# Optimization experiments

Hardware: AMD Instinct MI355X
Metric: run time of the kernel (lower is better)

## Reference

```python
import jax, jax.numpy as jnp
import numpy as np

D = 128; H = 8; L = 6; DFF = 512; EPS = 1e-5; ETA = 1e-3; MAXLEN = 5000


def layernorm(x, g, b):
    m = jnp.mean(x, -1, keepdims=True)
    v = jnp.mean((x - m) ** 2, -1, keepdims=True)
    return (x - m) / jnp.sqrt(v + EPS) * g + b


def mha(q_in, kv_in, Wi, bi, Wo, bo):
    # Wi: [3D, D] packed q/k/v projections (torch in_proj layout)
    dh = D // H
    q = q_in @ Wi[:D].T + bi[:D]
    k = kv_in @ Wi[D:2 * D].T + bi[D:2 * D]
    v = kv_in @ Wi[2 * D:].T + bi[2 * D:]
    B_, Lq, _ = q.shape
    Lk = k.shape[1]
    q = q.reshape(B_, Lq, H, dh)
    k = k.reshape(B_, Lk, H, dh)
    v = v.reshape(B_, Lk, H, dh)
    att = jax.nn.softmax(jnp.einsum('bqhd,bkhd->bhqk', q, k) / jnp.sqrt(jnp.asarray(dh, q.dtype)), axis=-1)
    o = jnp.einsum('bhqk,bkhd->bqhd', att, v).reshape(B_, Lq, D)
    return o @ Wo.T + bo


def posenc(x):
    pos = jnp.arange(MAXLEN, dtype=x.dtype)[:, None]
    div = jnp.exp(jnp.arange(0, D, 2, dtype=x.dtype) * (-jnp.log(jnp.asarray(10000.0, x.dtype)) / D))
    pe = jnp.zeros((MAXLEN, D), x.dtype).at[:, 0::2].set(jnp.sin(pos * div)).at[:, 1::2].set(jnp.cos(pos * div))
    # faithful to original: slices pe by x.size(0) which is the BATCH dim (batch_first tensors)
    return x + pe[: x.shape[0], None, :]


def reference(src, tgt, emb, femb_w, femb_b,
              enc_inw, enc_inb, enc_ow, enc_ob, enc_l1g, enc_l1b, enc_l2g, enc_l2b,
              enc_f1w, enc_f1b, enc_f2w, enc_f2b, enc_ng, enc_nb,
              dec_inw, dec_inb, dec_ow, dec_ob, dec_cinw, dec_cinb, dec_cow, dec_cob,
              dec_l1g, dec_l1b, dec_l2g, dec_l2b, dec_l3g, dec_l3b,
              dec_f1w, dec_f1b, dec_f2w, dec_f2b, dec_ng, dec_nb, fc_w, fc_b):
    scale = jnp.sqrt(jnp.asarray(D, jnp.float32))
    s = posenc(emb[src] * scale)                     # [B,S,D]
    t = posenc((tgt @ femb_w.T + femb_b) * scale)    # [B,T,D]
    mem = s
    for i in range(L):  # encoder (post-norm, ReLU, dropout=0 in eval)
        a = mha(mem, mem, enc_inw[i], enc_inb[i], enc_ow[i], enc_ob[i])
        mem = layernorm(mem + a, enc_l1g[i], enc_l1b[i])
        f = jax.nn.relu(mem @ enc_f1w[i].T + enc_f1b[i]) @ enc_f2w[i].T + enc_f2b[i]
        mem = layernorm(mem + f, enc_l2g[i], enc_l2b[i])
    mem = layernorm(mem, enc_ng, enc_nb)
    y = t
    for i in range(L):  # decoder
        a = mha(y, y, dec_inw[i], dec_inb[i], dec_ow[i], dec_ob[i])
        y = layernorm(y + a, dec_l1g[i], dec_l1b[i])
        c = mha(y, mem, dec_cinw[i], dec_cinb[i], dec_cow[i], dec_cob[i])
        y = layernorm(y + c, dec_l2g[i], dec_l2b[i])
        f = jax.nn.relu(y @ dec_f1w[i].T + dec_f1b[i]) @ dec_f2w[i].T + dec_f2b[i]
        y = layernorm(y + f, dec_l3g[i], dec_l3b[i])
    y = layernorm(y, dec_ng, dec_nb)
    out = y @ fc_w.T + fc_b  # [B,T,1]
    # nn-corrected TN parameter vector: vec + eta * nn_output (pre-final-contract)
    return tgt[..., 0] + ETA * out[..., 0]


def setup_inputs():
    B, S, T = 4, 100, 2048
    ks = iter(jax.random.split(jax.random.key(0), 64))

    def w(shape, s=0.02):
        return jax.random.normal(next(ks), shape, jnp.float32) * s

    inp = {}
    inp['src'] = jax.random.randint(next(ks), (B, S), 0, 2)
    inp['tgt'] = jax.random.normal(next(ks), (B, T, 1), jnp.float32)
    inp['emb'] = w((2, D), 1.0)
    inp['femb_w'] = w((D, 1)); inp['femb_b'] = jnp.zeros((D,))
    inp['enc_inw'] = w((L, 3 * D, D)); inp['enc_inb'] = jnp.zeros((L, 3 * D))
    inp['enc_ow'] = w((L, D, D)); inp['enc_ob'] = jnp.zeros((L, D))
    inp['enc_l1g'] = jnp.ones((L, D)); inp['enc_l1b'] = jnp.zeros((L, D))
    inp['enc_l2g'] = jnp.ones((L, D)); inp['enc_l2b'] = jnp.zeros((L, D))
    inp['enc_f1w'] = w((L, DFF, D)); inp['enc_f1b'] = jnp.zeros((L, DFF))
    inp['enc_f2w'] = w((L, D, DFF)); inp['enc_f2b'] = jnp.zeros((L, D))
    inp['enc_ng'] = jnp.ones((D,)); inp['enc_nb'] = jnp.zeros((D,))
    inp['dec_inw'] = w((L, 3 * D, D)); inp['dec_inb'] = jnp.zeros((L, 3 * D))
    inp['dec_ow'] = w((L, D, D)); inp['dec_ob'] = jnp.zeros((L, D))
    inp['dec_cinw'] = w((L, 3 * D, D)); inp['dec_cinb'] = jnp.zeros((L, 3 * D))
    inp['dec_cow'] = w((L, D, D)); inp['dec_cob'] = jnp.zeros((L, D))
    inp['dec_l1g'] = jnp.ones((L, D)); inp['dec_l1b'] = jnp.zeros((L, D))
    inp['dec_l2g'] = jnp.ones((L, D)); inp['dec_l2b'] = jnp.zeros((L, D))
    inp['dec_l3g'] = jnp.ones((L, D)); inp['dec_l3b'] = jnp.zeros((L, D))
    inp['dec_f1w'] = w((L, DFF, D)); inp['dec_f1b'] = jnp.zeros((L, DFF))
    inp['dec_f2w'] = w((L, D, DFF)); inp['dec_f2b'] = jnp.zeros((L, D))
    inp['dec_ng'] = jnp.ones((D,)); inp['dec_nb'] = jnp.zeros((D,))
    inp['fc_w'] = w((1, D)); inp['fc_b'] = jnp.zeros((1,))
    return inp
```

## Files before the change

### kernel.cpp

```cpp
#include <hip/hip_runtime.h>
#include <hip/hip_bf16.h>
#include <math.h>

#define B_ 4
#define S_ 100
#define T_ 2048
#define DM 128
#define NH 8
#define DH 16
#define NL 6
#define DFFN 512

#define SQRT_D 11.313708498984761f
#define LN10K  9.210340371976184f
#define QSCALE 0.36067376022224085f

typedef _Float16 v4h __attribute__((ext_vector_type(4)));
typedef _Float16 v8h __attribute__((ext_vector_type(8)));
typedef float    v4f __attribute__((ext_vector_type(4)));

__device__ __forceinline__ float fexp2(float x) { return __builtin_amdgcn_exp2f(x); }

__device__ __forceinline__ v4f mfma16(v4h a, v4h b, v4f c) {
    return __builtin_amdgcn_mfma_f32_16x16x16f16(a, b, c, 0, 0, 0);
}

__device__ __forceinline__ void gload_lds16(const void* g, void* l) {
    __builtin_amdgcn_global_load_lds(
        (const __attribute__((address_space(1))) unsigned int*)g,
        (__attribute__((address_space(3))) unsigned int*)l, 16, 0, 0);
}

__device__ __forceinline__ float pe_val(int pos, int d) {
    int i = d >> 1;
    float dv = __expf((float)i * (-2.0f * LN10K / 128.0f));
    float ang = (float)pos * dv;
    return (d & 1) ? __cosf(ang) : __sinf(ang);
}

__global__ __launch_bounds__(256) void conv_w(
    const float* __restrict__ p0, const float* __restrict__ p1,
    const float* __restrict__ p2, const float* __restrict__ p3,
    const float* __restrict__ p4, const float* __restrict__ p5,
    const float* __restrict__ p6, const float* __restrict__ p7,
    const float* __restrict__ p8, const float* __restrict__ p9,
    _Float16* __restrict__ out)
{
    int seg = blockIdx.y;
    const float* s; int sz; long off;
    switch (seg) {
        case 0: s = p0; sz = 294912; off = 0;       break;
        case 1: s = p1; sz = 98304;  off = 294912;  break;
        case 2: s = p2; sz = 393216; off = 393216;  break;
        case 3: s = p3; sz = 393216; off = 786432;  break;
        case 4: s = p4; sz = 294912; off = 1179648; break;
        case 5: s = p5; sz = 98304;  off = 1474560; break;
        case 6: s = p6; sz = 294912; off = 1572864; break;
        case 7: s = p7; sz = 98304;  off = 1867776; break;
        case 8: s = p8; sz = 393216; off = 1966080; break;
        default: s = p9; sz = 393216; off = 2359296; break;
    }
    int idx = (blockIdx.x * 256 + threadIdx.x) * 4;
    if (idx >= sz) return;
    float4 v = *(const float4*)(s + idx);
    v4h h = { (_Float16)v.x, (_Float16)v.y, (_Float16)v.z, (_Float16)v.w };
    *(v4h*)(out + off + idx) = h;
}

__global__ __launch_bounds__(256) void embed_src_kernel(
    const int* __restrict__ src, const float* __restrict__ emb,
    _Float16* __restrict__ outh)
{
    int idx = blockIdx.x * 256 + threadIdx.x;
    if (idx >= B_ * S_ * DM) return;
    int d = idx & 127;
    int row = idx >> 7;
    int b = row / S_;
    int tok = src[row];
    float v = emb[tok * DM + d] * SQRT_D + pe_val(b, d);
    outh[idx] = (_Float16)v;
}

__global__ __launch_bounds__(256) void embed_tgt_kernel(
    const float* __restrict__ tgt, const float* __restrict__ fw,
    const float* __restrict__ fb, _Float16* __restrict__ outh)
{
    int idx = blockIdx.x * 256 + threadIdx.x;
    if (idx >= B_ * T_ * DM) return;
    int d = idx & 127;
    int row = idx >> 7;
    int b = row >> 11;
    float v = (tgt[row] * fw[d] + fb[d]) * SQRT_D + pe_val(b, d);
    outh[idx] = (_Float16)v;
}

template<int MODE>
__global__ __launch_bounds__(256) void gemm_h(
    const _Float16* __restrict__ A, const _Float16* __restrict__ W,
    const float* __restrict__ bias,
    _Float16* __restrict__ Ch,
    _Float16* __restrict__ qo, _Float16* __restrict__ ko, _Float16* __restrict__ vo,
    int M, int N, int K, int L, int Lkp, int part_off, int Lshift,
    long zws, int zbs, long zks, long zvs)
{
    if (MODE == 2) {
        int zi = blockIdx.z;
        W += (size_t)zi * zws;
        bias += (size_t)zi * zbs;
        ko += (size_t)zi * zks;
        vo += (size_t)zi * zvs;
    }
    __shared__ _Float16 As[128][72];
    __shared__ _Float16 Ws[64][72];
    const int t = threadIdx.x;
    const int wave = t >> 6, lane = t & 63;
    const int col16 = lane & 15, grp = lane >> 4;
    const int row0 = blockIdx.x * 128, col0 = blockIdx.y * 64;
    const int wrow0 = (wave >> 1) * 64, wcol0 = (wave & 1) * 32;

    v4f acc[4][2];
    #pragma unroll
    for (int m = 0; m < 4; m++)
        #pragma unroll
        for (int n = 0; n < 2; n++) acc[m][n] = (v4f){0.f, 0.f, 0.f, 0.f};

    for (int k0 = 0; k0 < K; k0 += 64) {
        #pragma unroll
        for (int i = 0; i < 4; i++) {
            int id = i * 256 + t;
            int r = id >> 3, j = id & 7;
            int gr = min(row0 + r, M - 1);
            int4 v = *(const int4*)(A + (size_t)gr * K + k0 + j * 8);
            *(int4*)&As[r][j * 8] = v;
        }
        #pragma unroll
        for (int i = 0; i < 2; i++) {
            int id = i * 256 + t;
            int r = id >> 3, j = id & 7;
            int4 v = *(const int4*)(W + (size_t)(col0 + r) * K + k0 + j * 8);
            *(int4*)&Ws[r][j * 8] = v;
        }
        __syncthreads();
        #pragma unroll
        for (int kk = 0; kk < 4; kk++) {
            v4h a[4], bf[2];
            #pragma unroll
            for (int m = 0; m < 4; m++)
                a[m] = *(const v4h*)&As[wrow0 + m * 16 + col16][kk * 16 + grp * 4];
            #pragma unroll
            for (int n = 0; n < 2; n++)
                bf[n] = *(const v4h*)&Ws[wcol0 + n * 16 + col16][kk * 16 + grp * 4];
            #pragma unroll
            for (int m = 0; m < 4; m++)
                #pragma unroll
                for (int n = 0; n < 2; n++)
                    acc[m][n] = mfma16(a[m], bf[n], acc[m][n]);
        }
        __syncthreads();
    }

    #pragma unroll
    for (int n = 0; n < 2; n++) {
        int gcol = col0 + wcol0 + n * 16 + col16;
        float bv = bias[gcol];
        #pragma unroll
        for (int m = 0; m < 4; m++) {
            int rbase = row0 + wrow0 + m * 16 + grp * 4;
            #pragma unroll
            for (int r = 0; r < 4; r++) {
                int grow = rbase + r;
                if (grow >= M) continue;
                float v = acc[m][n][r] + bv;
                int pc = gcol + part_off;
                int part = pc >> 7;
                int h = (pc >> 4) & 7;
                int d = pc & 15;
                int b = Lshift ? (grow >> Lshift) : (grow / L);
                int pos = grow - b * L;
                int bh = b * NH + h;
                if (part == 0)
                    qo[((size_t)bh * L + pos) * 16 + d] = (_Float16)(v * QSCALE);
                else if (part == 1)
                    ko[((size_t)bh * L + pos) * 16 + d] = (_Float16)v;
                else
                    vo[((size_t)bh * 16 + d) * Lkp + pos] = (_Float16)v;
            }
        }
    }
}

template<int CROSS>
__global__ __launch_bounds__(128) void post_ln(
    const _Float16* __restrict__ A,
    const _Float16* __restrict__ po, const float* __restrict__ pm, const float* __restrict__ pl,
    const _Float16* __restrict__ Wo1, const float* __restrict__ bo1,
    const _Float16* __restrict__ resg,
    const float* __restrict__ g1, const float* __restrict__ bt1,
    const _Float16* __restrict__ Wq, const float* __restrict__ bq,
    const _Float16* __restrict__ KC_l, const _Float16* __restrict__ VC_l,
    const _Float16* __restrict__ Wo2, const float* __restrict__ bo2,
    const float* __restrict__ g2, const float* __restrict__ bt2,
    const _Float16* __restrict__ W1, const float* __restrict__ fb1,
    const _Float16* __restrict__ W2, const float* __restrict__ fb2,
    const float* __restrict__ g3, const float* __restrict__ bt3,
    _Float16* __restrict__ yout, int M)
{
    __shared__ _Float16 As[32][136];
    __shared__ _Float16 Ws[128][132];
    __shared__ _Float16 YL[32][136];
    __shared__ _Float16 QS[32][136];
    __shared__ _Float16 Khs[2][2048];
    __shared__ _Float16 Vhs[2][2048];
    __shared__ _Float16 W1s[64][136];
    __shared__ _Float16 Hs[32][72];
    __shared__ _Float16 W2s[128][72];
    const int t = threadIdx.x;
    const int wave = t >> 6, lane = t & 63;
    const int col16 = lane & 15, grp = lane >> 4;
    const int row0 = blockIdx.x * 32;
    const int rl = wave * 16 + grp * 4;

    v4f acc[8];
    #pragma unroll
    for (int n = 0; n < 8; n++) acc[n] = (v4f){0.f, 0.f, 0.f, 0.f};
    #pragma unroll
    for (int i = 0; i < 4; i++) {
        int id = i * 128 + t;
        int r = id >> 4, j = id & 15;
        int grow = min(row0 + r, M - 1);
        if (CROSS) {
            int dim0 = j * 8;
            int h = dim0 >> 4;
            int doff = dim0 & 8;
            int b = grow >> 11, q = grow & 2047;
            size_t i0 = ((size_t)(b * 2 + 0) * NH + h) * T_ + q;
            size_t i1 = ((size_t)(b * 2 + 1) * NH + h) * T_ + q;
            float m0 = pm[i0], m1 = pm[i1];
            float MM = fmaxf(m0, m1);
            float w0 = fexp2(m0 - MM) * pl[i0];
            float w1 = fexp2(m1 - MM) * pl[i1];
            float inv = 1.0f / (w0 + w1);
            w0 *= inv; w1 *= inv;
            v8h o0 = *(const v8h*)&po[i0 * 16 + doff];
            v8h o1 = *(const v8h*)&po[i1 * 16 + doff];
            v8h mrg;
            #pragma unroll
            for (int e = 0; e < 8; e++)
                mrg[e] = (_Float16)((float)o0[e] * w0 + (float)o1[e] * w1);
            *(v8h*)&As[r][j * 8] = mrg;
        } else {
            int4 v = *(const int4*)(A + (size_t)grow * DM + j * 8);
            *(int4*)&As[r][j * 8] = v;
        }
    }
    #pragma unroll
    for (int i = 0; i < 16; i++) {
        int id = i * 128 + t;
        int r = id >> 4, j = id & 15;
        int4 v = *(const int4*)(Wo1 + (size_t)r * DM + j * 8);
        *(int4*)&Ws[r][j * 8] = v;
    }
    __syncthreads();
    #pragma unroll
    for (int kk = 0; kk < 8; kk++) {
        v4h a = *(const v4h*)&As[wave * 16 + col16][kk * 16 + grp * 4];
        #pragma unroll
        for (int n = 0; n < 8; n++) {
            v4h bf = *(const v4h*)&Ws[n * 16 + col16][kk * 16 + grp * 4];
            acc[n] = mfma16(a, bf, acc[n]);
        }
    }
    {
        float bv[8], gv[8], btv[8];
        #pragma unroll
        for (int n = 0; n < 8; n++) {
            bv[n] = bo1[col16 + 16 * n];
            gv[n] = g1[col16 + 16 * n];
            btv[n] = bt1[col16 + 16 * n];
        }
        #pragma unroll
        for (int r = 0; r < 4; r++) {
            int grow = min(row0 + rl + r, M - 1);
            float x[8];
            float sum = 0.f;
            #pragma unroll
            for (int n = 0; n < 8; n++) {
                x[n] = acc[n][r] + bv[n] + (float)resg[(size_t)grow * DM + col16 + 16 * n];
                sum += x[n];
            }
            sum += __shfl_xor(sum, 1, 64);
            sum += __shfl_xor(sum, 2, 64);
            sum += __shfl_xor(sum, 4, 64);
            sum += __shfl_xor(sum, 8, 64);
            float mean = sum * (1.0f / 128.0f);
            float vs = 0.f;
            #pragma unroll
            for (int n = 0; n < 8; n++) { x[n] -= mean; vs += x[n] * x[n]; }
            vs += __shfl_xor(vs, 1, 64);
            vs += __shfl_xor(vs, 2, 64);
            vs += __shfl_xor(vs, 4, 64);
            vs += __shfl_xor(vs, 8, 64);
            float rstd = rsqrtf(vs * (1.0f / 128.0f) + 1e-5f);
            #pragma unroll
            for (int n = 0; n < 8; n++)
                YL[rl + r][col16 + 16 * n] = (_Float16)(x[n] * rstd * gv[n] + btv[n]);
        }
    }
    __syncthreads();

    if (CROSS) {
        v4f qacc[8];
        #pragma unroll
        for (int n = 0; n < 8; n++) qacc[n] = (v4f){0.f, 0.f, 0.f, 0.f};
        #pragma unroll
        for (int i = 0; i < 16; i++) {
            int id = i * 128 + t;
            int r = id >> 4, j = id & 15;
            int4 v = *(const int4*)(Wq + (size_t)r * DM + j * 8);
            *(int4*)&Ws[r][j * 8] = v;
        }
        __syncthreads();
        #pragma unroll
        for (int kk = 0; kk < 8; kk++) {
            v4h a = *(const v4h*)&YL[wave * 16 + col16][kk * 16 + grp * 4];
            #pragma unroll
            for (int n = 0; n < 8; n++) {
                v4h bf = *(const v4h*)&Ws[n * 16 + col16][kk * 16 + grp * 4];
                qacc[n] = mfma16(a, bf, qacc[n]);
            }
        }
        __syncthreads();
        #pragma unroll
        for (int n = 0; n < 8; n++) {
            float bb = bq[n * 16 + col16];
            #pragma unroll
            for (int r = 0; r < 4; r++)
                QS[rl + r][n * 16 + col16] = (_Float16)((qacc[n][r] + bb) * QSCALE);
        }

        const int b = row0 >> 11;
        const char* kbB = (const char*)(KC_l + (size_t)(b * NH) * S_ * DH);
        const char* vbB = (const char*)(VC_l + (size_t)(b * NH) * DH * 128);
        for (int h = 0; h < NH; h += 2) {
            __syncthreads();
            #pragma unroll
            for (int s = 0; s < 2; s++) {
                int hh = h + s;
                #pragma unroll
                for (int rd = 0; rd < 2; rd++) {
                    int dstB = rd * 2048 + wave * 1024 + lane * 16;
                    int krow = dstB >> 5;
                    int half = (dstB >> 4) & 1;
                    gload_lds16(kbB + (long)hh * 3200 + (long)krow * 32 +
                                ((half ^ ((krow >> 2) & 1)) << 4),
                                (char*)&Khs[s][0] + rd * 2048 + wave * 1024);
                }
                #pragma unroll
                for (int rd = 0; rd < 2; rd++) {
                    int dstB = rd * 2048 + wave * 1024 + lane * 16;
                    int vd = dstB >> 8;
                    int inoff = dstB & 255;
                    gload_lds16(vbB + (long)hh * 4096 + (long)vd * 256 +
                                (inoff ^ ((vd & 7) << 4)),
                                (char*)&Vhs[s][0] + rd * 2048 + wave * 1024);
                }
            }
            __syncthreads();

            #pragma unroll
            for (int s = 0; s < 2; s++) {
                int hh = h + s;
                v4h q_frag = *(const v4h*)&QS[wave * 16 + col16][hh * 16 + grp * 4];
                const int kxor = (col16 & 4) << 2;
                v4f s4[7];
                #pragma unroll
                for (int sub = 0; sub < 7; sub++) {
                    int koff = ((sub * 16 + col16) << 5) + ((grp * 8) ^ kxor);
                    v4h k_frag = *(const v4h*)((const char*)&Khs[s][0] + koff);
                    s4[sub] = mfma16(k_frag, q_frag, (v4f){0.f, 0.f, 0.f, 0.f});
                }
                #pragma unroll
                for (int r = 0; r < 4; r++) {
                    int key = 96 + grp * 4 + r;
                    if (key >= S_) s4[6][r] = -1e30f;
                }
                float mx = -1e30f;
                #pragma unroll
                for (int sub = 0; sub < 7; sub++)
                    #pragma unroll
                    for (int r = 0; r < 4; r++) mx = fmaxf(mx, s4[sub][r]);
                mx = fmaxf(mx, __shfl_xor(mx, 16, 64));
                mx = fmaxf(mx, __shfl_xor(mx, 32, 64));
                float l = 0.f;
                float p[7][4];
                #pragma unroll
                for (int sub = 0; sub < 7; sub++)
                    #pragma unroll
                    for (int r = 0; r < 4; r++) {
                        p[sub][r] = fexp2(s4[sub][r] - mx);
                        l += p[sub][r];
                    }
                l += __shfl_xor(l, 16, 64);
                l += __shfl_xor(l, 32, 64);
                float inv = 1.0f / l;
                v4f o = {0.f, 0.f, 0.f, 0.f};
                #pragma unroll
                for (int sub = 0; sub < 7; sub++) {
                    v4h ph = { (_Float16)(p[sub][0] * inv), (_Float16)(p[sub][1] * inv),
                               (_Float16)(p[sub][2] * inv), (_Float16)(p[sub][3] * inv) };
                    int vbyte = (col16 << 8) + ((sub * 32 + grp * 8) ^ ((col16 & 7) << 4));
                    v4h vt = *(const v4h*)((const char*)&Vhs[s][0] + vbyte);
                    o = mfma16(vt, ph, o);
                }
                #pragma unroll
                for (int r = 0; r < 4; r++)
                    QS[wave * 16 + col16][hh * 16 + grp * 4 + r] = (_Float16)o[r];
            }
        }
        __syncthreads();

        v4f ac2[8];
        #pragma unroll
        for (int n = 0; n < 8; n++) ac2[n] = (v4f){0.f, 0.f, 0.f, 0.f};
        #pragma unroll
        for (int i = 0; i < 16; i++) {
            int id = i * 128 + t;
            int r = id >> 4, j = id & 15;
            int4 v = *(const int4*)(Wo2 + (size_t)r * DM + j * 8);
            *(int4*)&Ws[r][j * 8] = v;
        }
        __syncthreads();
        #pragma unroll
        for (int kk = 0; kk < 8; kk++) {
            v4h a = *(const v4h*)&QS[wave * 16 + col16][kk * 16 + grp * 4];
            #pragma unroll
            for (int n = 0; n < 8; n++) {
                v4h bf = *(const v4h*)&Ws[n * 16 + col16][kk * 16 + grp * 4];
                ac2[n] = mfma16(a, bf, ac2[n]);
            }
        }
        {
            float bv[8], gv[8], btv[8];
            #pragma unroll
            for (int n = 0; n < 8; n++) {
                bv[n] = bo2[col16 + 16 * n];
                gv[n] = g2[col16 + 16 * n];
                btv[n] = bt2[col16 + 16 * n];
            }
            #pragma unroll
            for (int r = 0; r < 4; r++) {
                float x[8];
                float sum = 0.f;
                #pragma unroll
                for (int n = 0; n < 8; n++) {
                    x[n] = ac2[n][r] + bv[n] + (float)YL[rl + r][col16 + 16 * n];
                    sum += x[n];
                }
                sum += __shfl_xor(sum, 1, 64);
                sum += __shfl_xor(sum, 2, 64);
                sum += __shfl_xor(sum, 4, 64);
                sum += __shfl_xor(sum, 8, 64);
                float mean = sum * (1.0f / 128.0f);
                float vs = 0.f;
                #pragma unroll
                for (int n = 0; n < 8; n++) { x[n] -= mean; vs += x[n] * x[n]; }
                vs += __shfl_xor(vs, 1, 64);
                vs += __shfl_xor(vs, 2, 64);
                vs += __shfl_xor(vs, 4, 64);
                vs += __shfl_xor(vs, 8, 64);
                float rstd = rsqrtf(vs * (1.0f / 128.0f) + 1e-5f);
                #pragma unroll
                for (int n = 0; n < 8; n++)
                    YL[rl + r][col16 + 16 * n] = (_Float16)(x[n] * rstd * gv[n] + btv[n]);
            }
        }
        __syncthreads();
    }

    v4f oacc[8];
    #pragma unroll
    for (int n = 0; n < 8; n++) oacc[n] = (v4f){0.f, 0.f, 0.f, 0.f};
    for (int hc = 0; hc < 8; hc++) {
        #pragma unroll
        for (int rd = 0; rd < 8; rd++) {
            int id = rd * 128 + t;
            int r = id >> 4, j = id & 15;
            int4 v = *(const int4*)(W1 + (size_t)(hc * 64 + r) * DM + j * 8);
            *(int4*)&W1s[r][j * 8] = v;
        }
        #pragma unroll
        for (int rd = 0; rd < 8; rd++) {
            int id = rd * 128 + t;
            int r = id >> 3, j = id & 7;
            int4 v = *(const int4*)(W2 + (size_t)r * DFFN + hc * 64 + j * 8);
            *(int4*)&W2s[r][j * 8] = v;
        }
        __syncthreads();
        v4f hacc[4];
        #pragma unroll
        for (int n = 0; n < 4; n++) hacc[n] = (v4f){0.f, 0.f, 0.f, 0.f};
        #pragma unroll
        for (int kk = 0; kk < 8; kk++) {
            v4h a = *(const v4h*)&YL[wave * 16 + col16][kk * 16 + grp * 4];
            #pragma unroll
            for (int n = 0; n < 4; n++) {
                v4h bf = *(const v4h*)&W1s[n * 16 + col16][kk * 16 + grp * 4];
                hacc[n] = mfma16(a, bf, hacc[n]);
            }
        }
        #pragma unroll
        for (int n = 0; n < 4; n++) {
            float bb = fb1[hc * 64 + n * 16 + col16];
            #pragma unroll
            for (int r = 0; r < 4; r++) {
                float h = fmaxf(hacc[n][r] + bb, 0.f);
                Hs[rl + r][n * 16 + col16] = (_Float16)h;
            }
        }
        #pragma unroll
        for (int kk = 0; kk < 4; kk++) {
            v4h a = *(const v4h*)&Hs[wave * 16 + col16][kk * 16 + grp * 4];
            #pragma unroll
            for (int n = 0; n < 8; n++) {
                v4h bf = *(const v4h*)&W2s[n * 16 + col16][kk * 16 + grp * 4];
                oacc[n] = mfma16(a, bf, oacc[n]);
            }
        }
        __syncthreads();
    }
    {
        float bv[8], gv[8], btv[8];
        #pragma unroll
        for (int n = 0; n < 8; n++) {
            bv[n] = fb2[col16 + 16 * n];
            gv[n] = g3[col16 + 16 * n];
            btv[n] = bt3[col16 + 16 * n];
        }
        #pragma unroll
        for (int r = 0; r < 4; r++) {
            int row = row0 + rl + r;
            float x[8];
            float sum = 0.f;
            #pragma unroll
            for (int n = 0; n < 8; n++) {
                x[n] = oacc[n][r] + bv[n] + (float)YL[rl + r][col16 + 16 * n];
                sum += x[n];
            }
            sum += __shfl_xor(sum, 1, 64);
            sum += __shfl_xor(sum, 2, 64);
            sum += __shfl_xor(sum, 4, 64);
            sum += __shfl_xor(sum, 8, 64);
            float mean = sum * (1.0f / 128.0f);
            float vs = 0.f;
            #pragma unroll
            for (int n = 0; n < 8; n++) { x[n] -= mean; vs += x[n] * x[n]; }
            vs += __shfl_xor(vs, 1, 64);
            vs += __shfl_xor(vs, 2, 64);
            vs += __shfl_xor(vs, 4, 64);
            vs += __shfl_xor(vs, 8, 64);
            float rstd = rsqrtf(vs * (1.0f / 128.0f) + 1e-5f);
            if (row < M) {
                #pragma unroll
                for (int n = 0; n < 8; n++) {
                    float o = x[n] * rstd * gv[n] + btv[n];
                    yout[(size_t)row * DM + col16 + 16 * n] = (_Float16)o;
                }
            }
        }
    }
}

template<int FINAL>
__global__ __launch_bounds__(256, 6) void attn_p3(
    const _Float16* __restrict__ qh, const _Float16* __restrict__ kh,
    const _Float16* __restrict__ vth, _Float16* __restrict__ outh,
    _Float16* __restrict__ po, float* __restrict__ pm, float* __restrict__ pl,
    int Lq, int Lk, int Lkp, int NS)
{
    __shared__ _Float16 KV[2][2048];
    const int zb = blockIdx.z;
    const int b = zb / NS, split = zb - b * NS;
    const int h = blockIdx.y;
    const int wave = threadIdx.x >> 6, lane = threadIdx.x & 63;
    const int col16 = lane & 15, grp = lane >> 4;
    const int bh = b * NH + h;
    const int qrow = (blockIdx.x * 4 + wave) * 16 + col16;
    const int qcl = min(qrow, Lq - 1);

    v4h q_frag = *(const v4h*)(qh + ((size_t)bh * Lq + qcl) * 16 + grp * 4);
    const char* kbB = (const char*)(kh + (size_t)bh * Lk * 16);
    const char* vbB = (const char*)(vth + (size_t)bh * 16 * Lkp);
    const int LkpB = Lkp * 2;

    const int kvLen = Lk / NS;
    const int kv0 = split * kvLen;
    const int kvEnd = kv0 + kvLen;

    const int krow = wave * 32 + (lane >> 1);
    const long ksrc_off = (long)krow * 32 + (((lane & 1) ^ ((krow >> 2) & 1)) << 4);
    const int vd = (wave & 1) * 8 + (lane >> 3);
    const long vsrc_off = (long)vd * LkpB + (((lane & 7) * 16) ^ ((vd & 7) << 4));
    char* ldsK = (char*)&KV[0][0] + wave * 1024;
    char* ldsV = (char*)&KV[0][0] + 2048 + (wave & 1) * 1024;

    auto stage = [&](int buf, int kc) {
        if (wave < 2)
            gload_lds16(kbB + (long)kc * 32 + ksrc_off, ldsK + buf * 4096);
        else
            gload_lds16(vbB + (long)kc * 2 + vsrc_off, ldsV + buf * 4096);
    };

    const int kxor = (col16 & 4) << 2;

    float m = -1e30f;
    v4f l4 = {0.f, 0.f, 0.f, 0.f};
    v4f oa = {0.f, 0.f, 0.f, 0.f}, ob = {0.f, 0.f, 0.f, 0.f};

    stage(0, kv0);
    __syncthreads();

    int nChunks = (kvLen + 63) >> 6;
    int cur = 0;
    for (int ci = 0; ci < nChunks; ci++, cur ^= 1) {
        int kc = kv0 + ci * 64;
        if (ci + 1 < nChunks) stage(cur ^ 1, kc + 64);

        const char* base = (const char*)&KV[cur][0];
        v4f s4[4];
        #pragma unroll
        for (int sub = 0; sub < 4; sub++) {
            int koff = ((sub * 16 + col16) << 5) + ((grp * 8) ^ kxor);
            v4h k_frag = *(const v4h*)(base + koff);
            s4[sub] = mfma16(k_frag, q_frag, (v4f){0.f, 0.f, 0.f, 0.f});
        }
        if (kc + 64 > kvEnd) {
            #pragma unroll
            for (int sub = 0; sub < 4; sub++)
                #pragma unroll
                for (int r = 0; r < 4; r++) {
                    int key = kc + sub * 16 + grp * 4 + r;
                    if (key >= kvEnd) s4[sub][r] = -1e30f;
                }
        }
        float c0 = fmaxf(fmaxf(s4[0][0], s4[0][1]), fmaxf(s4[0][2], s4[0][3]));
        float c1 = fmaxf(fmaxf(s4[1][0], s4[1][1]), fmaxf(s4[1][2], s4[1][3]));
        float c2 = fmaxf(fmaxf(s4[2][0], s4[2][1]), fmaxf(s4[2][2], s4[2][3]));
        float c3 = fmaxf(fmaxf(s4[3][0], s4[3][1]), fmaxf(s4[3][2], s4[3][3]));
        float cm = fmaxf(fmaxf(c0, c1), fmaxf(c2, c3));
        if (__any(cm > m + 8.0f)) {
            float nm = fmaxf(cm, m);
            nm = fmaxf(nm, __shfl_xor(nm, 16, 64));
            nm = fmaxf(nm, __shfl_xor(nm, 32, 64));
            float corr = fexp2(m - nm);
            l4[0] *= corr; l4[1] *= corr; l4[2] *= corr; l4[3] *= corr;
            oa[0] *= corr; oa[1] *= corr; oa[2] *= corr; oa[3] *= corr;
            ob[0] *= corr; ob[1] *= corr; ob[2] *= corr; ob[3] *= corr;
            m = nm;
        }
        v4h ph[4];
        #pragma unroll
        for (int sub = 0; sub < 4; sub++) {
            float p0 = fexp2(s4[sub][0] - m);
            float p1 = fexp2(s4[sub][1] - m);
            float p2 = fexp2(s4[sub][2] - m);
            float p3 = fexp2(s4[sub][3] - m);
            l4[0] += p0; l4[1] += p1; l4[2] += p2; l4[3] += p3;
            ph[sub] = (v4h){ (_Float16)p0, (_Float16)p1, (_Float16)p2, (_Float16)p3 };
        }
        #pragma unroll
        for (int sub = 0; sub < 4; sub++) {
            int vbyte = 2048 + (col16 << 7) + ((sub * 32 + grp * 8) ^ ((col16 & 7) << 4));
            v4h vt_frag = *(const v4h*)(base + vbyte);
            if (sub & 2)
                ob = mfma16(vt_frag, ph[sub], ob);
            else
                oa = mfma16(vt_frag, ph[sub], oa);
        }
        __syncthreads();
    }

    float l = (l4[0] + l4[1]) + (l4[2] + l4[3]);
    l += __shfl_xor(l, 16, 64);
    l += __shfl_xor(l, 32, 64);
    float inv = 1.0f / l;
    v4f o_acc = {oa[0] + ob[0], oa[1] + ob[1], oa[2] + ob[2], oa[3] + ob[3]};
    if (qrow < Lq) {
        v4h ov = { (_Float16)(o_acc[0] * inv), (_Float16)(o_acc[1] * inv),
                   (_Float16)(o_acc[2] * inv), (_Float16)(o_acc[3] * inv) };
        if (FINAL) {
            *(v4h*)(outh + ((size_t)b * Lq + qrow) * DM + h * DH + grp * 4) = ov;
        } else {
            size_t pidx = ((size_t)zb * NH + h) * Lq + qrow;
            *(v4h*)(po + pidx * 16 + grp * 4) = ov;
            if (grp == 0) { pm[pidx] = m; pl[pidx] = l; }
        }
    }
}

__global__ __launch_bounds__(256) void ln_h(
    _Float16* __restrict__ y, const float* __restrict__ g,
    const float* __restrict__ bta, int M)
{
    int row = blockIdx.x * 4 + (threadIdx.x >> 6);
    int lane = threadIdx.x & 63;
    if (row >= M) return;
    _Float16* yr = y + (size_t)row * DM;
    float x0 = (float)yr[lane], x1 = (float)yr[lane + 64];
    float sum = x0 + x1;
    #pragma unroll
    for (int off = 32; off > 0; off >>= 1) sum += __shfl_xor(sum, off, 64);
    float mean = sum * (1.0f / 128.0f);
    float d0 = x0 - mean, d1 = x1 - mean;
    float vs = d0 * d0 + d1 * d1;
    #pragma unroll
    for (int off = 32; off > 0; off >>= 1) vs += __shfl_xor(vs, off, 64);
    float rstd = rsqrtf(vs * (1.0f / 128.0f) + 1e-5f);
    yr[lane]      = (_Float16)(d0 * rstd * g[lane]      + bta[lane]);
    yr[lane + 64] = (_Float16)(d1 * rstd * g[lane + 64] + bta[lane + 64]);
}

__global__ __launch_bounds__(256) void final_ln_kernel(
    const _Float16* __restrict__ y, const float* __restrict__ tgt,
    const float* __restrict__ g, const float* __restrict__ bta,
    const float* __restrict__ fcw, const float* __restrict__ fcb,
    float* __restrict__ out)
{
    int row = blockIdx.x * 4 + (threadIdx.x >> 6);
    int lane = threadIdx.x & 63;
    const _Float16* yr = y + (size_t)row * DM;
    float x0 = (float)yr[lane], x1 = (float)yr[lane + 64];
    float sum = x0 + x1;
    #pragma unroll
    for (int off = 32; off > 0; off >>= 1) sum += __shfl_xor(sum, off, 64);
    float mean = sum * (1.0f / 128.0f);
    float d0 = x0 - mean, d1 = x1 - mean;
    float vs = d0 * d0 + d1 * d1;
    #pragma unroll
    for (int off = 32; off > 0; off >>= 1) vs += __shfl_xor(vs, off, 64);
    float rstd = rsqrtf(vs * (1.0f / 128.0f) + 1e-5f);
    float o0 = d0 * rstd * g[lane]      + bta[lane];
    float o1 = d1 * rstd * g[lane + 64] + bta[lane + 64];
    float a = o0 * fcw[lane] + o1 * fcw[lane + 64];
    #pragma unroll
    for (int off = 32; off > 0; off >>= 1) a += __shfl_xor(a, off, 64);
    if (lane == 0) out[row] = tgt[row] + 1.0e-3f * (a + fcb[0]);
}

extern "C" void kernel_launch(void* const* d_in, const int* in_sizes, int n_in,
                              void* d_out, int out_size, void* d_ws, size_t ws_size,
                              hipStream_t stream)
{
    (void)in_sizes; (void)n_in; (void)out_size; (void)ws_size;
    const int*   src     = (const int*)  d_in[0];
    const float* tgt     = (const float*)d_in[1];
    const float* emb     = (const float*)d_in[2];
    const float* femb_w  = (const float*)d_in[3];
    const float* femb_b  = (const float*)d_in[4];
    const float* enc_inw = (const float*)d_in[5];
    const float* enc_inb = (const float*)d_in[6];
    const float* enc_ow  = (const float*)d_in[7];
    const float* enc_ob  = (const float*)d_in[8];
    const float* enc_l1g = (const float*)d_in[9];
    const float* enc_l1b = (const float*)d_in[10];
    const float* enc_l2g = (const float*)d_in[11];
    const float* enc_l2b = (const float*)d_in[12];
    const float* enc_f1w = (const float*)d_in[13];
    const float* enc_f1b = (const float*)d_in[14];
    const float* enc_f2w = (const float*)d_in[15];
    const float* enc_f2b = (const float*)d_in[16];
    const float* enc_ng  = (const float*)d_in[17];
    const float* enc_nb  = (const float*)d_in[18];
    const float* dec_inw = (const float*)d_in[19];
    const float* dec_inb = (const float*)d_in[20];
    const float* dec_ow  = (const float*)d_in[21];
    const float* dec_ob  = (const float*)d_in[22];
    const float* dec_cinw= (const float*)d_in[23];
    const float* dec_cinb= (const float*)d_in[24];
    const float* dec_cow = (const float*)d_in[25];
    const float* dec_cob = (const float*)d_in[26];
    const float* dec_l1g = (const float*)d_in[27];
    const float* dec_l1b = (const float*)d_in[28];
    const float* dec_l2g = (const float*)d_in[29];
    const float* dec_l2b = (const float*)d_in[30];
    const float* dec_l3g = (const float*)d_in[31];
    const float* dec_l3b = (const float*)d_in[32];
    const float* dec_f1w = (const float*)d_in[33];
    const float* dec_f1b = (const float*)d_in[34];
    const float* dec_f2w = (const float*)d_in[35];
    const float* dec_f2b = (const float*)d_in[36];
    const float* dec_ng  = (const float*)d_in[37];
    const float* dec_nb  = (const float*)d_in[38];
    const float* fc_w    = (const float*)d_in[39];
    const float* fc_b    = (const float*)d_in[40];

    float* ws = (float*)d_ws;
    float* pm   = ws;
    float* pl   = ws + 131072;
    _Float16* hb = (_Float16*)(ws + 262144);
    _Float16* mem_h  = hb;
    _Float16* ybuf_h = hb + 51200;
    _Float16* aout_h = hb + 1099776;
    _Float16* wh     = hb + 2148352;
    _Float16* po     = hb + 4900864;
    _Float16* QH     = hb + 11192320;
    _Float16* KH     = hb + 12240896;
    _Float16* VTH    = hb + 13289472;
    _Float16* KC     = hb + 14338048;
    _Float16* VC     = hb + 14645248;

    const long W_ENC_INW = 0,       W_ENC_OW = 294912,  W_ENC_F1W = 393216,  W_ENC_F2W = 786432;
    const long W_DEC_INW = 1179648, W_DEC_OW = 1474560, W_DEC_CINW = 1572864, W_DEC_COW = 1867776;
    const long W_DEC_F1W = 1966080, W_DEC_F2W = 2359296;

    conv_w<<<dim3(384, 10), 256, 0, stream>>>(enc_inw, enc_ow, enc_f1w, enc_f2w,
                                              dec_inw, dec_ow, dec_cinw, dec_cow,
                                              dec_f1w, dec_f2w, wh);

    embed_src_kernel<<<200, 256, 0, stream>>>(src, emb, mem_h);
    for (int i = 0; i < NL; i++) {
        gemm_h<2><<<dim3(4, 6), 256, 0, stream>>>(mem_h, wh + W_ENC_INW + i * 49152, enc_inb + i * 384,
            nullptr, QH, KH, VTH, 400, 384, 128, 100, 128, 0, 0, 0, 0, 0, 0);
        attn_p3<1><<<dim3(2, NH, B_), 256, 0, stream>>>(QH, KH, VTH, aout_h,
            nullptr, nullptr, nullptr, 100, 100, 128, 1);
        post_ln<0><<<13, 128, 0, stream>>>(aout_h,
            nullptr, nullptr, nullptr,
            wh + W_ENC_OW + i * 16384, enc_ob + i * 128,
            mem_h, enc_l1g + i * 128, enc_l1b + i * 128,
            nullptr, nullptr, nullptr, nullptr, nullptr, nullptr, nullptr, nullptr,
            wh + W_ENC_F1W + i * 65536, enc_f1b + i * 512,
            wh + W_ENC_F2W + i * 65536, enc_f2b + i * 128,
            enc_l2g + i * 128, enc_l2b + i * 128,
            mem_h, 400);
    }
    ln_h<<<100, 256, 0, stream>>>(mem_h, enc_ng, enc_nb, 400);
    gemm_h<2><<<dim3(4, 4, 6), 256, 0, stream>>>(mem_h, wh + W_DEC_CINW + 16384, dec_cinb + 128,
        nullptr, nullptr, KC, VC, 400, 256, 128, 100, 128, 128, 0,
        49152, 384, 51200, 65536);

    embed_tgt_kernel<<<4096, 256, 0, stream>>>(tgt, femb_w, femb_b, ybuf_h);
    for (int i = 0; i < NL; i++) {
        gemm_h<2><<<dim3(64, 6), 256, 0, stream>>>(ybuf_h, wh + W_DEC_INW + i * 49152, dec_inb + i * 384,
            nullptr, QH, KH, VTH, 8192, 384, 128, 2048, 2048, 0, 11, 0, 0, 0, 0);
        attn_p3<0><<<dim3(32, NH, B_ * 2), 256, 0, stream>>>(QH, KH, VTH, nullptr,
            po, pm, pl, 2048, 2048, 2048, 2);
        post_ln<1><<<256, 128, 0, stream>>>(nullptr,
            po, pm, pl,
            wh + W_DEC_OW + i * 16384, dec_ob + i * 128,
            ybuf_h, dec_l1g + i * 128, dec_l1b + i * 128,
            wh + W_DEC_CINW + i * 49152, dec_cinb + i * 384,
            KC + i * 51200, VC + i * 65536,
            wh + W_DEC_COW + i * 16384, dec_cob + i * 128,
            dec_l2g + i * 128, dec_l2b + i * 128,
            wh + W_DEC_F1W + i * 65536, dec_f1b + i * 512,
            wh + W_DEC_F2W + i * 65536, dec_f2b + i * 128,
            dec_l3g + i * 128, dec_l3b + i * 128,
            ybuf_h, 8192);
    }
    final_ln_kernel<<<2048, 256, 0, stream>>>(ybuf_h, tgt, dec_ng, dec_nb, fc_w, fc_b, (float*)d_out);
}
```

Baseline: 698.0 us.

## Double-buffer cross-attention K/V staging and register-prefetch FFN weight chunks

Cross-attention now handles one head per iteration and issues the async K/V loads for the next head into the other LDS buffer before computing the current one. This overlaps global-to-LDS transfer with the QK/softmax/PV work. The FFN loop preloads the next W1/W2 chunk into registers while the current chunk is being computed, hiding global load latency. The cost is extra register pressure (16 int4 held per thread) and one barrier per head instead of one per pair of heads.

```diff
diff --git a/kernel.cpp b/kernel.cpp
--- a/kernel.cpp
+++ b/kernel.cpp
@@ -188,6 +188,28 @@
         }
     }
 }
+
+#define STAGEC(hh, s)                                                          \
+    {                                                                          \
+        _Pragma("unroll")                                                      \
+        for (int rd = 0; rd < 2; rd++) {                                       \
+            int dstB = rd * 2048 + wave * 1024 + lane * 16;                    \
+            int krow = dstB >> 5;                                              \
+            int half = (dstB >> 4) & 1;                                        \
+            gload_lds16(kbB + (long)(hh) * 3200 + (long)krow * 32 +            \
+                        ((half ^ ((krow >> 2) & 1)) << 4),                     \
+                        (char*)&Khs[s][0] + rd * 2048 + wave * 1024);          \
+        }                                                                      \
+        _Pragma("unroll")                                                      \
+        for (int rd = 0; rd < 2; rd++) {                                      \
+            int dstB = rd * 2048 + wave * 1024 + lane * 16;                    \
+            int vd = dstB >> 8;                                                \
+            int inoff = dstB & 255;                                            \
+            gload_lds16(vbB + (long)(hh) * 4096 + (long)vd * 256 +             \
+                        (inoff ^ ((vd & 7) << 4)),                             \
+                        (char*)&Vhs[s][0] + rd * 2048 + wave * 1024);          \
+        }                                                                      \
+    }
 
 template<int CROSS>
 __global__ __launch_bounds__(128) void post_ln(
@@ -341,83 +363,58 @@
         const int b = row0 >> 11;
         const char* kbB = (const char*)(KC_l + (size_t)(b * NH) * S_ * DH);
         const char* vbB = (const char*)(VC_l + (size_t)(b * NH) * DH * 128);
-        for (int h = 0; h < NH; h += 2) {
-            __syncthreads();
-            #pragma unroll
-            for (int s = 0; s < 2; s++) {
-                int hh = h + s;
+        STAGEC(0, 0);
+        __syncthreads();
+        for (int h = 0; h < NH; h++) {
+            int s = h & 1;
+            if (h < NH - 1) STAGEC(h + 1, (h + 1) & 1);
+            v4h q_frag = *(const v4h*)&QS[wave * 16 + col16][h * 16 + grp * 4];
+            const int kxor = (col16 & 4) << 2;
+            v4f s4[7];
+            #pragma unroll
+            for (int sub = 0; sub < 7; sub++) {
+                int koff = ((sub * 16 + col16) << 5) + ((grp * 8) ^ kxor);
+                v4h k_frag = *(const v4h*)((const char*)&Khs[s][0] + koff);
+                s4[sub] = mfma16(k_frag, q_frag, (v4f){0.f, 0.f, 0.f, 0.f});
+            }
+            #pragma unroll
+            for (int r = 0; r < 4; r++) {
+                int key = 96 + grp * 4 + r;
+                if (key >= S_) s4[6][r] = -1e30f;
+            }
+            float mx = -1e30f;
+            #pragma unroll
+            for (int sub = 0; sub < 7; sub++)
                 #pragma unroll
-                for (int rd = 0; rd < 2; rd++) {
-                    int dstB = rd * 2048 + wave * 1024 + lane * 16;
-                    int krow = dstB >> 5;
-                    int half = (dstB >> 4) & 1;
-                    gload_lds16(kbB + (long)hh * 3200 + (long)krow * 32 +
-                                ((half ^ ((krow >> 2) & 1)) << 4),
-                                (char*)&Khs[s][0] + rd * 2048 + wave * 1024);
-                }
-                #pragma unroll
-                for (int rd = 0; rd < 2; rd++) {
-                    int dstB = rd * 2048 + wave * 1024 + lane * 16;
-                    int vd = dstB >> 8;
-                    int inoff = dstB & 255;
-                    gload_lds16(vbB + (long)hh * 4096 + (long)vd * 256 +
-                                (inoff ^ ((vd & 7) << 4)),
-                                (char*)&Vhs[s][0] + rd * 2048 + wave * 1024);
-                }
-            }
-            __syncthreads();
-
-            #pragma unroll
-            for (int s = 0; s < 2; s++) {
-                int hh = h + s;
-                v4h q_frag = *(const v4h*)&QS[wave * 16 + col16][hh * 16 + grp * 4];
-                const int kxor = (col16 & 4) << 2;
-                v4f s4[7];
-                #pragma unroll
-                for (int sub = 0; sub < 7; sub++) {
-                    int koff = ((sub * 16 + col16) << 5) + ((grp * 8) ^ kxor);
-                    v4h k_frag = *(const v4h*)((const char*)&Khs[s][0] + koff);
-                    s4[sub] = mfma16(k_frag, q_frag, (v4f){0.f, 0.f, 0.f, 0.f});
-                }
+                for (int r = 0; r < 4; r++) mx = fmaxf(mx, s4[sub][r]);
+            mx = fmaxf(mx, __shfl_xor(mx, 16, 64));
+            mx = fmaxf(mx, __shfl_xor(mx, 32, 64));
+            float l = 0.f;
+            float p[7][4];
+            #pragma unroll
+            for (int sub = 0; sub < 7; sub++)
                 #pragma unroll
                 for (int r = 0; r < 4; r++) {
-                    int key = 96 + grp * 4 + r;
-                    if (key >= S_) s4[6][r] = -1e30f;
+                    p[sub][r] = fexp2(s4[sub][r] - mx);
+                    l += p[sub][r];
                 }
-                float mx = -1e30f;
-                #pragma unroll
-                for (int sub = 0; sub < 7; sub++)
-                    #pragma unroll
-                    for (int r = 0; r < 4; r++) mx = fmaxf(mx, s4[sub][r]);
-                mx = fmaxf(mx, __shfl_xor(mx, 16, 64));
-                mx = fmaxf(mx, __shfl_xor(mx, 32, 64));
-                float l = 0.f;
-                float p[7][4];
-                #pragma unroll
-                for (int sub = 0; sub < 7; sub++)
-                    #pragma unroll
-                    for (int r = 0; r < 4; r++) {
-                        p[sub][r] = fexp2(s4[sub][r] - mx);
-                        l += p[sub][r];
-                    }
-                l += __shfl_xor(l, 16, 64);
-                l += __shfl_xor(l, 32, 64);
-                float inv = 1.0f / l;
-                v4f o = {0.f, 0.f, 0.f, 0.f};
-                #pragma unroll
-                for (int sub = 0; sub < 7; sub++) {
-                    v4h ph = { (_Float16)(p[sub][0] * inv), (_Float16)(p[sub][1] * inv),
-                               (_Float16)(p[sub][2] * inv), (_Float16)(p[sub][3] * inv) };
-                    int vbyte = (col16 << 8) + ((sub * 32 + grp * 8) ^ ((col16 & 7) << 4));
-                    v4h vt = *(const v4h*)((const char*)&Vhs[s][0] + vbyte);
-                    o = mfma16(vt, ph, o);
-                }
-                #pragma unroll
-                for (int r = 0; r < 4; r++)
-                    QS[wave * 16 + col16][hh * 16 + grp * 4 + r] = (_Float16)o[r];
-            }
-        }
-        __syncthreads();
+            l += __shfl_xor(l, 16, 64);
+            l += __shfl_xor(l, 32, 64);
+            float inv = 1.0f / l;
+            v4f o = {0.f, 0.f, 0.f, 0.f};
+            #pragma unroll
+            for (int sub = 0; sub < 7; sub++) {
+                v4h ph = { (_Float16)(p[sub][0] * inv), (_Float16)(p[sub][1] * inv),
+                           (_Float16)(p[sub][2] * inv), (_Float16)(p[sub][3] * inv) };
+                int vbyte = (col16 << 8) + ((sub * 32 + grp * 8) ^ ((col16 & 7) << 4));
+                v4h vt = *(const v4h*)((const char*)&Vhs[s][0] + vbyte);
+                o = mfma16(vt, ph, o);
+            }
+            #pragma unroll
+            for (int r = 0; r < 4; r++)
+                QS[wave * 16 + col16][h * 16 + grp * 4 + r] = (_Float16)o[r];
+            __syncthreads();
+        }
 
         v4f ac2[8];
         #pragma unroll
@@ -480,22 +477,41 @@
     v4f oacc[8];
     #pragma unroll
     for (int n = 0; n < 8; n++) oacc[n] = (v4f){0.f, 0.f, 0.f, 0.f};
+    int4 w1r[8], w2r[8];
+    #pragma unroll
+    for (int i = 0; i < 8; i++) {
+        int id = i * 128 + t;
+        w1r[i] = *(const int4*)(W1 + (size_t)(id >> 4) * DM + (id & 15) * 8);
+    }
+    #pragma unroll
+    for (int i = 0; i < 8; i++) {
+        int id = i * 128 + t;
+        w2r[i] = *(const int4*)(W2 + (size_t)(id >> 3) * DFFN + (id & 7) * 8);
+    }
     for (int hc = 0; hc < 8; hc++) {
         #pragma unroll
-        for (int rd = 0; rd < 8; rd++) {
-            int id = rd * 128 + t;
-            int r = id >> 4, j = id & 15;
-            int4 v = *(const int4*)(W1 + (size_t)(hc * 64 + r) * DM + j * 8);
-            *(int4*)&W1s[r][j * 8] = v;
-        }
-        #pragma unroll
-        for (int rd = 0; rd < 8; rd++) {
-            int id = rd * 128 + t;
-            int r = id >> 3, j = id & 7;
-            int4 v = *(const int4*)(W2 + (size_t)r * DFFN + hc * 64 + j * 8);
-            *(int4*)&W2s[r][j * 8] = v;
-        }
-        __syncthreads();
+        for (int i = 0; i < 8; i++) {
+            int id = i * 128 + t;
+            *(int4*)&W1s[id >> 4][(id & 15) * 8] = w1r[i];
+        }
+        #pragma unroll
+        for (int i = 0; i < 8; i++) {
+            int id = i * 128 + t;
+            *(int4*)&W2s[id >> 3][(id & 7) * 8] = w2r[i];
+        }
+        __syncthreads();
+        if (hc < 7) {
+            #pragma unroll
+            for (int i = 0; i < 8; i++) {
+                int id = i * 128 + t;
+                w1r[i] = *(const int4*)(W1 + (size_t)((hc + 1) * 64 + (id >> 4)) * DM + (id & 15) * 8);
+            }
+            #pragma unroll
+            for (int i = 0; i < 8; i++) {
+                int id = i * 128 + t;
+                w2r[i] = *(const int4*)(W2 + (size_t)(id >> 3) * DFFN + (hc + 1) * 64 + (id & 7) * 8);
+            }
+        }
         v4f hacc[4];
         #pragma unroll
         for (int n = 0; n < 4; n++) hacc[n] = (v4f){0.f, 0.f, 0.f, 0.f};
```

After: 853.3 us. 1.22x slower.

## Double-buffer FFN weight chunks via async global-to-LDS loads with XOR swizzle

Applied to the files above, without the earlier changes.

The FFN loop in post_ln now stages W1/W2 chunks with direct global-to-LDS loads into a double-buffered shared pool, prefetching chunk hc+1 while computing chunk hc. The rows are XOR-swizzled to avoid bank conflicts, and the old Ws array aliases the same pool. The goal is to hide weight-load latency and drop the register round trip through VGPRs. It relies on the existing end-of-iteration barrier to order buffer reuse, and it enlarges shared memory, which may lower occupancy.

```diff
diff --git a/kernel.cpp b/kernel.cpp
--- a/kernel.cpp
+++ b/kernel.cpp
@@ -189,6 +189,24 @@
     }
 }
 
+#define STAGEE(hcv, bv)                                                        \
+    {                                                                          \
+        char* w1base = (char*)(POOL + (bv) * 8192);                            \
+        char* w2base = (char*)(POOL + 16384 + (bv) * 8192);                    \
+        _Pragma("unroll")                                                      \
+        for (int i = 0; i < 8; i++) {                                          \
+            int dB = i * 2048 + wave * 1024 + lane * 16;                       \
+            int r1 = dB >> 8, c1 = dB & 255;                                   \
+            gload_lds16((const char*)W1 + (size_t)((hcv) * 64 + r1) * 256 +    \
+                        (c1 ^ ((r1 & 7) << 4)),                                \
+                        w1base + i * 2048 + wave * 1024);                      \
+            int r2 = dB >> 7, c2 = dB & 127;                                   \
+            gload_lds16((const char*)W2 + (size_t)r2 * 1024 + (hcv) * 128 +    \
+                        (c2 ^ ((r2 & 7) << 4)),                                \
+                        w2base + i * 2048 + wave * 1024);                      \
+        }                                                                      \
+    }
+
 template<int CROSS>
 __global__ __launch_bounds__(128) void post_ln(
     const _Float16* __restrict__ A,
@@ -206,14 +224,13 @@
     _Float16* __restrict__ yout, int M)
 {
     __shared__ _Float16 As[32][136];
-    __shared__ _Float16 Ws[128][132];
+    __shared__ __align__(16) _Float16 POOL[32768];
     __shared__ _Float16 YL[32][136];
     __shared__ _Float16 QS[32][136];
     __shared__ _Float16 Khs[2][2048];
     __shared__ _Float16 Vhs[2][2048];
-    __shared__ _Float16 W1s[64][136];
     __shared__ _Float16 Hs[32][72];
-    __shared__ _Float16 W2s[128][72];
+    _Float16 (*Ws)[132] = (_Float16 (*)[132])POOL;
     const int t = threadIdx.x;
     const int wave = t >> 6, lane = t & 63;
     const int col16 = lane & 15, grp = lane >> 4;
@@ -480,22 +497,14 @@
     v4f oacc[8];
     #pragma unroll
     for (int n = 0; n < 8; n++) oacc[n] = (v4f){0.f, 0.f, 0.f, 0.f};
+    const int kx = (col16 & 7) << 4;
+    STAGEE(0, 0);
+    __syncthreads();
     for (int hc = 0; hc < 8; hc++) {
-        #pragma unroll
-        for (int rd = 0; rd < 8; rd++) {
-            int id = rd * 128 + t;
-            int r = id >> 4, j = id & 15;
-            int4 v = *(const int4*)(W1 + (size_t)(hc * 64 + r) * DM + j * 8);
-            *(int4*)&W1s[r][j * 8] = v;
-        }
-        #pragma unroll
-        for (int rd = 0; rd < 8; rd++) {
-            int id = rd * 128 + t;
-            int r = id >> 3, j = id & 7;
-            int4 v = *(const int4*)(W2 + (size_t)r * DFFN + hc * 64 + j * 8);
-            *(int4*)&W2s[r][j * 8] = v;
-        }
-        __syncthreads();
+        int cur = hc & 1;
+        if (hc < 7) STAGEE(hc + 1, cur ^ 1);
+        const char* w1c = (const char*)(POOL + cur * 8192);
+        const char* w2c = (const char*)(POOL + 16384 + cur * 8192);
         v4f hacc[4];
         #pragma unroll
         for (int n = 0; n < 4; n++) hacc[n] = (v4f){0.f, 0.f, 0.f, 0.f};
@@ -504,7 +513,7 @@
             v4h a = *(const v4h*)&YL[wave * 16 + col16][kk * 16 + grp * 4];
             #pragma unroll
             for (int n = 0; n < 4; n++) {
-                v4h bf = *(const v4h*)&W1s[n * 16 + col16][kk * 16 + grp * 4];
+                v4h bf = *(const v4h*)(w1c + (n * 16 + col16) * 256 + ((kk * 32 + grp * 8) ^ kx));
                 hacc[n] = mfma16(a, bf, hacc[n]);
             }
         }
@@ -522,7 +531,7 @@
             v4h a = *(const v4h*)&Hs[wave * 16 + col16][kk * 16 + grp * 4];
             #pragma unroll
             for (int n = 0; n < 8; n++) {
-                v4h bf = *(const v4h*)&W2s[n * 16 + col16][kk * 16 + grp * 4];
+                v4h bf = *(const v4h*)(w2c + (n * 16 + col16) * 128 + ((kk * 32 + grp * 8) ^ kx));
                 oacc[n] = mfma16(a, bf, oacc[n]);
             }
         }
```

Result: slower. 750.1 us (+7.5%).
